# Performance work log

Measured on AMD Instinct MI355X. Metric: run time of the kernel, lower is better.

## Reference

```python
import jax, jax.numpy as jnp
import numpy as np

NUM_MEMORIES = 4096
HIDDEN_DIM = 64
TEMPERATURE = 0.5
SHRINK_THRES = 0.0025
EPS = 1e-12


def _l2_normalize(v, axis=-1):
    # matches torch F.normalize: v / max(||v||_2, eps)
    n = jnp.sqrt(jnp.sum(v * v, axis=axis, keepdims=True))
    return v / jnp.maximum(n, EPS)


def _hard_shrink_relu(w, lambd):
    # relu(w - lambd) * w / (|w - lambd| + eps)
    d = w - lambd
    return jax.nn.relu(d) * w / (jnp.abs(d) + EPS)


def setup_inputs() -> dict:
    key = jax.random.key(0)
    kx, km = jax.random.split(key)
    x = jax.random.normal(kx, (16, 2048, HIDDEN_DIM), dtype=jnp.float32)
    # xavier_uniform for (num_memories, hidden_dim)
    bound = float(np.sqrt(6.0 / (NUM_MEMORIES + HIDDEN_DIM)))
    memories = jax.random.uniform(km, (NUM_MEMORIES, HIDDEN_DIM), dtype=jnp.float32,
                                  minval=-bound, maxval=bound)
    return {"x": x, "memories": memories}


def reference(x, memories):
    # cosine similarity addressing
    x_n = _l2_normalize(x, axis=-1)                      # [B,S,D]
    m_n = _l2_normalize(memories, axis=-1)               # [M,D]
    logits = jnp.einsum('bsd,md->bsm', x_n, m_n)         # [B,S,M]
    weight = jax.nn.softmax(logits / TEMPERATURE, axis=-1)
    # hard-shrink sparsification + L1 renormalization
    weight = _hard_shrink_relu(weight, SHRINK_THRES)
    l1 = jnp.sum(jnp.abs(weight), axis=-1, keepdims=True)
    weight = weight / jnp.maximum(l1, EPS)
    read = jnp.einsum('bsm,md->bsd', weight, memories)   # [B,S,D]
    return read, weight
```

## Files before the change

### kernel.cpp

```cpp
#include <hip/hip_runtime.h>
#include <hip/hip_bf16.h>


#define NM 4096
#define HD 64
#define NROWS 32768

typedef short bf16x8 __attribute__((ext_vector_type(8)));
typedef float f32x4  __attribute__((ext_vector_type(4)));

__global__ __launch_bounds__(256) void prep_rows(const float* __restrict__ src,
                                                 ushort* __restrict__ dst,
                                                 float scale,
                                                 float* __restrict__ Mv) {
    if (blockIdx.x == 0 && threadIdx.x < 64) Mv[threadIdx.x] = 0.0f;
    const int wave = threadIdx.x >> 6, lane = threadIdx.x & 63;
    const long row = (long)blockIdx.x * 4 + wave;
    float v = src[row * HD + lane];
    float s = v * v;
#pragma unroll
    for (int o = 32; o; o >>= 1) s += __shfl_xor(s, o, 64);
    const float inv = scale / fmaxf(sqrtf(s), 1e-12f);
    __hip_bfloat16 h = __float2bfloat16(v * inv);
    dst[row * HD + lane] = *reinterpret_cast<ushort*>(&h);
}

__global__ __launch_bounds__(256) void prep_m_swz(const float* __restrict__ mem,
                                                  ushort* __restrict__ mbs,
                                                  float* __restrict__ Mv) {
    __shared__ float sM[4][64];
    const int wave = threadIdx.x >> 6, lane = threadIdx.x & 63;
    const int row = blockIdx.x * 4 + wave;
    float v = mem[row * HD + lane];
    float s = v * v;
#pragma unroll
    for (int o = 32; o; o >>= 1) s += __shfl_xor(s, o, 64);
    const float inv = 1.0f / fmaxf(sqrtf(s), 1e-12f);
    const float nv = v * inv;
    __hip_bfloat16 h = __float2bfloat16(nv);
    const int t = row >> 4, c = row & 15;
    const int k = lane;
    const int f = k >> 5, q = (k >> 3) & 3, j = k & 7;
    mbs[(long)t * 1024 + f * 512 + (q * 16 + c) * 8 + j] =
        *reinterpret_cast<ushort*>(&h);
    sM[wave][lane] = nv;
    __syncthreads();
    if (wave == 0)
        atomicAdd(&Mv[lane],
                  sM[0][lane] + sM[1][lane] + sM[2][lane] + sM[3][lane]);
}

__global__ __launch_bounds__(256, 4) void k_zero(const float* __restrict__ x,
                                                 const float* __restrict__ Mv,
                                                 const ushort* __restrict__ xb,
                                                 const ushort* __restrict__ mbs,
                                                 const float* __restrict__ mem,
                                                 float* __restrict__ out_w,
                                                 float* __restrict__ out_read) {
    const int tid = threadIdx.x;
    const int wv = tid >> 6, lane = tid & 63;
    const int m0 = blockIdx.x * 16;

    __shared__ float sS[4][16];
    __shared__ float sL[4][16];
    __shared__ int   sFail[4];
    __shared__ float sred[4][16][64];

    {
        const int r16 = lane >> 4;
        const int k16 = lane & 15;
        const long row = (long)m0 + wv * 4 + r16;
        const float4 xv = *(const float4*)(x + row * HD + k16 * 4);
        const float4 mv = *(const float4*)(Mv + k16 * 4);
        float dot = xv.x * mv.x + xv.y * mv.y + xv.z * mv.z + xv.w * mv.w;
        float nn  = xv.x * xv.x + xv.y * xv.y + xv.z * xv.z + xv.w * xv.w;
#pragma unroll
        for (int o = 1; o < 16; o <<= 1) {
            dot += __shfl_xor(dot, o, 64);
            nn  += __shfl_xor(nn,  o, 64);
        }
        const bool pass = dot >= -573.44f * fmaxf(sqrtf(nn), 1e-12f);
        const unsigned long long bal = __ballot(!pass);
        if (lane == 0) sFail[wv] = (bal != 0ull);
    }

    const float4 z4 = make_float4(0.0f, 0.0f, 0.0f, 0.0f);
    float4* base = (float4*)(out_w + (long)m0 * NM);
#pragma unroll 8
    for (int it = 0; it < 64; it++)
        base[it * 256 + tid] = z4;
    ((float4*)(out_read + (long)m0 * HD))[tid] = z4;

    __syncthreads();
    if (!(sFail[0] | sFail[1] | sFail[2] | sFail[3])) return;

    const int q = lane >> 4, c = lane & 15;
    const int nbase = wv * 1024;
    const bf16x8 a0 = *(const bf16x8*)(xb + (long)(m0 + c) * HD + q * 8);
    const bf16x8 a1 = *(const bf16x8*)(xb + (long)(m0 + c) * HD + q * 8 + 32);
    const ushort* mstrip = mbs + (long)(wv * 64) * 1024;

    float sm[4] = {0.0f, 0.0f, 0.0f, 0.0f};
    for (int i = 0; i < 64; i++) {
        const ushort* mc = mstrip + (long)i * 1024 + lane * 8;
        const bf16x8 b0 = *(const bf16x8*)(mc);
        const bf16x8 b1 = *(const bf16x8*)(mc + 512);
        f32x4 t = {0.0f, 0.0f, 0.0f, 0.0f};
        t = __builtin_amdgcn_mfma_f32_16x16x32_bf16(a0, b0, t, 0, 0, 0);
        t = __builtin_amdgcn_mfma_f32_16x16x32_bf16(a1, b1, t, 0, 0, 0);
#pragma unroll
        for (int r = 0; r < 4; r++) sm[r] += __expf(t[r]);
    }
#pragma unroll
    for (int o = 1; o < 16; o <<= 1)
#pragma unroll
        for (int r = 0; r < 4; r++) sm[r] += __shfl_xor(sm[r], o, 64);
    if (c == 0)
#pragma unroll
        for (int r = 0; r < 4; r++) sS[wv][q * 4 + r] = sm[r];
    __syncthreads();
    float rS[4];
#pragma unroll
    for (int r = 0; r < 4; r++)
        rS[r] = 1.0f / (sS[0][q * 4 + r] + sS[1][q * 4 + r] +
                        sS[2][q * 4 + r] + sS[3][q * 4 + r]);

    float l1[4] = {0.0f, 0.0f, 0.0f, 0.0f};
    for (int i = 0; i < 64; i++) {
        const ushort* mc = mstrip + (long)i * 1024 + lane * 8;
        const bf16x8 b0 = *(const bf16x8*)(mc);
        const bf16x8 b1 = *(const bf16x8*)(mc + 512);
        f32x4 t = {0.0f, 0.0f, 0.0f, 0.0f};
        t = __builtin_amdgcn_mfma_f32_16x16x32_bf16(a0, b0, t, 0, 0, 0);
        t = __builtin_amdgcn_mfma_f32_16x16x32_bf16(a1, b1, t, 0, 0, 0);
#pragma unroll
        for (int r = 0; r < 4; r++) {
            float w = __expf(t[r]) * rS[r];
            float d = w - 0.0025f;
            l1[r] += __fdividef(fmaxf(d, 0.0f) * w, fabsf(d) + 1e-12f);
        }
    }
#pragma unroll
    for (int o = 1; o < 16; o <<= 1)
#pragma unroll
        for (int r = 0; r < 4; r++) l1[r] += __shfl_xor(l1[r], o, 64);
    if (c == 0)
#pragma unroll
        for (int r = 0; r < 4; r++) sL[wv][q * 4 + r] = l1[r];
    __syncthreads();
    float rL[4];
#pragma unroll
    for (int r = 0; r < 4; r++)
        rL[r] = 1.0f / fmaxf(sL[0][q * 4 + r] + sL[1][q * 4 + r] +
                             sL[2][q * 4 + r] + sL[3][q * 4 + r], 1e-12f);

    float racc[16];
#pragma unroll
    for (int r = 0; r < 16; r++) racc[r] = 0.0f;
    float* wbase = out_w + (long)(m0 + q * 4) * NM + c;
    for (int i = 0; i < 64; i++) {
        const int n0 = nbase + i * 16;
        const ushort* mc = mstrip + (long)i * 1024 + lane * 8;
        const bf16x8 b0 = *(const bf16x8*)(mc);
        const bf16x8 b1 = *(const bf16x8*)(mc + 512);
        f32x4 t = {0.0f, 0.0f, 0.0f, 0.0f};
        t = __builtin_amdgcn_mfma_f32_16x16x32_bf16(a0, b0, t, 0, 0, 0);
        t = __builtin_amdgcn_mfma_f32_16x16x32_bf16(a1, b1, t, 0, 0, 0);
        float wf[4];
#pragma unroll
        for (int r = 0; r < 4; r++) {
            float w  = __expf(t[r]) * rS[r];
            float d  = w - 0.0025f;
            float sh = __fdividef(fmaxf(d, 0.0f) * w, fabsf(d) + 1e-12f);
            wf[r] = sh * rL[r];
            wbase[(long)r * NM + n0] = wf[r];
        }
        const bool nz = (wf[0] != 0.0f) | (wf[1] != 0.0f) |
                        (wf[2] != 0.0f) | (wf[3] != 0.0f);
        unsigned long long mask = __ballot(nz);
        while (mask) {
            const int j = __ffsll((long long)mask) - 1;
            mask &= (mask - 1);
            const int qj = j >> 4, cj = j & 15;
            float b0v = __shfl(wf[0], j, 64), b1v = __shfl(wf[1], j, 64);
            float b2v = __shfl(wf[2], j, 64), b3v = __shfl(wf[3], j, 64);
            const float mv = mem[(long)(n0 + cj) * HD + lane];
            switch (qj) {
                case 0: racc[0]  += b0v * mv; racc[1]  += b1v * mv;
                        racc[2]  += b2v * mv; racc[3]  += b3v * mv; break;
                case 1: racc[4]  += b0v * mv; racc[5]  += b1v * mv;
                        racc[6]  += b2v * mv; racc[7]  += b3v * mv; break;
                case 2: racc[8]  += b0v * mv; racc[9]  += b1v * mv;
                        racc[10] += b2v * mv; racc[11] += b3v * mv; break;
                default: racc[12] += b0v * mv; racc[13] += b1v * mv;
                         racc[14] += b2v * mv; racc[15] += b3v * mv; break;
            }
        }
    }

#pragma unroll
    for (int r = 0; r < 16; r++) sred[wv][r][lane] = racc[r];
    __syncthreads();
#pragma unroll
    for (int rr = 0; rr < 4; rr++) {
        const int row = wv * 4 + rr;
        const float v = sred[0][row][lane] + sred[1][row][lane] +
                        sred[2][row][lane] + sred[3][row][lane];
        out_read[(long)(m0 + row) * HD + lane] = v;
    }
}

extern "C" void kernel_launch(void* const* d_in, const int* in_sizes, int n_in,
                              void* d_out, int out_size, void* d_ws, size_t ws_size,
                              hipStream_t stream) {
    const float* x   = (const float*)d_in[0];
    const float* mem = (const float*)d_in[1];
    ushort* xb       = (ushort*)d_ws;
    ushort* mbs      = xb + (long)NROWS * HD;
    float*  Mv       = (float*)(mbs + (long)NM * HD);
    float* out_read  = (float*)d_out;
    float* out_w     = out_read + (long)NROWS * HD;

    prep_rows<<<NROWS / 4, 256, 0, stream>>>(x, xb, 2.0f, Mv);
    prep_m_swz<<<NM / 4, 256, 0, stream>>>(mem, mbs, Mv);
    k_zero<<<NROWS / 16, 256, 0, stream>>>(x, Mv, xb, mbs, mem, out_w, out_read);
}
```

Measured before the change: 563.2 us.

## Drop bf16 prep kernels and use per-wave early-exit with scalar fallback

Removes the x bf16 normalisation kernel and the swizzled memory-bank kernel. A single small kernel now writes per-block partial sums of the normalised memories to a buffer, replacing the atomics into a shared mean vector. The main kernel rebuilds the mean vector per wave, runs the all-weights-below-threshold check per wave instead of per block, and zero-fills only that wave's rows, so no block-level syncs are needed. The rare fallback path loses its MFMA version and becomes a plain fp32 scalar loop, which would be far slower if any row ever fails the check.

```diff
diff --git a/kernel.cpp b/kernel.cpp
--- a/kernel.cpp
+++ b/kernel.cpp
@@ -1,212 +1,141 @@
 #include <hip/hip_runtime.h>
-#include <hip/hip_bf16.h>
 
 
 #define NM 4096
 #define HD 64
 #define NROWS 32768
 
-typedef short bf16x8 __attribute__((ext_vector_type(8)));
-typedef float f32x4  __attribute__((ext_vector_type(4)));
-
-__global__ __launch_bounds__(256) void prep_rows(const float* __restrict__ src,
-                                                 ushort* __restrict__ dst,
-                                                 float scale,
-                                                 float* __restrict__ Mv) {
-    if (blockIdx.x == 0 && threadIdx.x < 64) Mv[threadIdx.x] = 0.0f;
+__global__ __launch_bounds__(256) void k_m(const float* __restrict__ mem,
+                                           float* __restrict__ P) {
+    __shared__ float sM[4][64];
     const int wave = threadIdx.x >> 6, lane = threadIdx.x & 63;
-    const long row = (long)blockIdx.x * 4 + wave;
-    float v = src[row * HD + lane];
-    float s = v * v;
+    float acc = 0.0f;
 #pragma unroll
-    for (int o = 32; o; o >>= 1) s += __shfl_xor(s, o, 64);
-    const float inv = scale / fmaxf(sqrtf(s), 1e-12f);
-    __hip_bfloat16 h = __float2bfloat16(v * inv);
-    dst[row * HD + lane] = *reinterpret_cast<ushort*>(&h);
+    for (int s = 0; s < 16; s++) {
+        const int i = blockIdx.x * 64 + wave * 16 + s;
+        const float v = mem[i * HD + lane];
+        float ss = v * v;
+#pragma unroll
+        for (int o = 32; o; o >>= 1) ss += __shfl_xor(ss, o, 64);
+        acc += v / fmaxf(sqrtf(ss), 1e-12f);
+    }
+    sM[wave][lane] = acc;
+    __syncthreads();
+    if (wave == 0)
+        P[blockIdx.x * 64 + lane] =
+            sM[0][lane] + sM[1][lane] + sM[2][lane] + sM[3][lane];
 }
 
-__global__ __launch_bounds__(256) void prep_m_swz(const float* __restrict__ mem,
-                                                  ushort* __restrict__ mbs,
-                                                  float* __restrict__ Mv) {
-    __shared__ float sM[4][64];
-    const int wave = threadIdx.x >> 6, lane = threadIdx.x & 63;
-    const int row = blockIdx.x * 4 + wave;
-    float v = mem[row * HD + lane];
-    float s = v * v;
-#pragma unroll
-    for (int o = 32; o; o >>= 1) s += __shfl_xor(s, o, 64);
-    const float inv = 1.0f / fmaxf(sqrtf(s), 1e-12f);
-    const float nv = v * inv;
-    __hip_bfloat16 h = __float2bfloat16(nv);
-    const int t = row >> 4, c = row & 15;
-    const int k = lane;
-    const int f = k >> 5, q = (k >> 3) & 3, j = k & 7;
-    mbs[(long)t * 1024 + f * 512 + (q * 16 + c) * 8 + j] =
-        *reinterpret_cast<ushort*>(&h);
-    sM[wave][lane] = nv;
-    __syncthreads();
-    if (wave == 0)
-        atomicAdd(&Mv[lane],
-                  sM[0][lane] + sM[1][lane] + sM[2][lane] + sM[3][lane]);
-}
-
-__global__ __launch_bounds__(256, 4) void k_zero(const float* __restrict__ x,
-                                                 const float* __restrict__ Mv,
-                                                 const ushort* __restrict__ xb,
-                                                 const ushort* __restrict__ mbs,
-                                                 const float* __restrict__ mem,
-                                                 float* __restrict__ out_w,
-                                                 float* __restrict__ out_read) {
+__global__ __launch_bounds__(256) void k_zero(const float* __restrict__ x,
+                                              const float* __restrict__ P,
+                                              const float* __restrict__ mem,
+                                              float* __restrict__ out_w,
+                                              float* __restrict__ out_read) {
     const int tid = threadIdx.x;
     const int wv = tid >> 6, lane = tid & 63;
-    const int m0 = blockIdx.x * 16;
+    const long rowbase = (long)blockIdx.x * 16 + wv * 4;
+    const int r16 = lane >> 4, k16 = lane & 15;
 
-    __shared__ float sS[4][16];
-    __shared__ float sL[4][16];
-    __shared__ int   sFail[4];
-    __shared__ float sred[4][16][64];
-
-    {
-        const int r16 = lane >> 4;
-        const int k16 = lane & 15;
-        const long row = (long)m0 + wv * 4 + r16;
-        const float4 xv = *(const float4*)(x + row * HD + k16 * 4);
-        const float4 mv = *(const float4*)(Mv + k16 * 4);
-        float dot = xv.x * mv.x + xv.y * mv.y + xv.z * mv.z + xv.w * mv.w;
-        float nn  = xv.x * xv.x + xv.y * xv.y + xv.z * xv.z + xv.w * xv.w;
+    float4 mv = make_float4(0.0f, 0.0f, 0.0f, 0.0f);
 #pragma unroll
-        for (int o = 1; o < 16; o <<= 1) {
-            dot += __shfl_xor(dot, o, 64);
-            nn  += __shfl_xor(nn,  o, 64);
-        }
-        const bool pass = dot >= -573.44f * fmaxf(sqrtf(nn), 1e-12f);
-        const unsigned long long bal = __ballot(!pass);
-        if (lane == 0) sFail[wv] = (bal != 0ull);
+    for (int b = 0; b < 16; b++) {
+        const float4 p = *(const float4*)(P + (r16 * 16 + b) * 64 + k16 * 4);
+        mv.x += p.x; mv.y += p.y; mv.z += p.z; mv.w += p.w;
+    }
+#pragma unroll
+    for (int o = 16; o < 64; o <<= 1) {
+        mv.x += __shfl_xor(mv.x, o, 64);
+        mv.y += __shfl_xor(mv.y, o, 64);
+        mv.z += __shfl_xor(mv.z, o, 64);
+        mv.w += __shfl_xor(mv.w, o, 64);
     }
 
-    const float4 z4 = make_float4(0.0f, 0.0f, 0.0f, 0.0f);
-    float4* base = (float4*)(out_w + (long)m0 * NM);
+    const long crow = rowbase + r16;
+    const float4 xv = *(const float4*)(x + crow * HD + k16 * 4);
+    float dot = xv.x * mv.x + xv.y * mv.y + xv.z * mv.z + xv.w * mv.w;
+    float nn  = xv.x * xv.x + xv.y * xv.y + xv.z * xv.z + xv.w * xv.w;
+#pragma unroll
+    for (int o = 1; o < 16; o <<= 1) {
+        dot += __shfl_xor(dot, o, 64);
+        nn  += __shfl_xor(nn,  o, 64);
+    }
+    const bool pass = dot >= -573.44f * fmaxf(sqrtf(nn), 1e-12f);
+
+    if (__ballot(!pass) == 0ull) {
+        const float4 z4 = make_float4(0.0f, 0.0f, 0.0f, 0.0f);
+        ((float4*)(out_read + rowbase * HD))[lane] = z4;
+        float4* base = (float4*)(out_w + rowbase * NM);
 #pragma unroll 8
-    for (int it = 0; it < 64; it++)
-        base[it * 256 + tid] = z4;
-    ((float4*)(out_read + (long)m0 * HD))[tid] = z4;
+        for (int it = 0; it < 64; it++)
+            base[it * 64 + lane] = z4;
+        return;
+    }
 
-    __syncthreads();
-    if (!(sFail[0] | sFail[1] | sFail[2] | sFail[3])) return;
+    for (int r = 0; r < 4; r++) {
+        const long rw = rowbase + r;
+        const float v = x[rw * HD + lane];
+        float ss = v * v;
+#pragma unroll
+        for (int o = 32; o; o >>= 1) ss += __shfl_xor(ss, o, 64);
+        const float xh = v * (2.0f / fmaxf(sqrtf(ss), 1e-12f));
 
-    const int q = lane >> 4, c = lane & 15;
-    const int nbase = wv * 1024;
-    const bf16x8 a0 = *(const bf16x8*)(xb + (long)(m0 + c) * HD + q * 8);
-    const bf16x8 a1 = *(const bf16x8*)(xb + (long)(m0 + c) * HD + q * 8 + 32);
-    const ushort* mstrip = mbs + (long)(wv * 64) * 1024;
+        float S = 0.0f;
+        for (int j = 0; j < 64; j++) {
+            const int i = j * 64 + lane;
+            float dp = 0.0f, nm = 0.0f;
+            for (int k = 0; k < 64; k++) {
+                const float mk = mem[(long)i * HD + k];
+                dp += __shfl(xh, k, 64) * mk;
+                nm += mk * mk;
+            }
+            const float t = dp / fmaxf(sqrtf(nm), 1e-12f);
+            S += __expf(t);
+        }
+#pragma unroll
+        for (int o = 1; o < 64; o <<= 1) S += __shfl_xor(S, o, 64);
+        const float rS = 1.0f / S;
 
-    float sm[4] = {0.0f, 0.0f, 0.0f, 0.0f};
-    for (int i = 0; i < 64; i++) {
-        const ushort* mc = mstrip + (long)i * 1024 + lane * 8;
-        const bf16x8 b0 = *(const bf16x8*)(mc);
-        const bf16x8 b1 = *(const bf16x8*)(mc + 512);
-        f32x4 t = {0.0f, 0.0f, 0.0f, 0.0f};
-        t = __builtin_amdgcn_mfma_f32_16x16x32_bf16(a0, b0, t, 0, 0, 0);
-        t = __builtin_amdgcn_mfma_f32_16x16x32_bf16(a1, b1, t, 0, 0, 0);
+        float l1 = 0.0f;
+        for (int j = 0; j < 64; j++) {
+            const int i = j * 64 + lane;
+            float dp = 0.0f, nm = 0.0f;
+            for (int k = 0; k < 64; k++) {
+                const float mk = mem[(long)i * HD + k];
+                dp += __shfl(xh, k, 64) * mk;
+                nm += mk * mk;
+            }
+            const float t = dp / fmaxf(sqrtf(nm), 1e-12f);
+            const float w = __expf(t) * rS;
+            const float d = w - 0.0025f;
+            l1 += fmaxf(d, 0.0f) * w / (fabsf(d) + 1e-12f);
+        }
 #pragma unroll
-        for (int r = 0; r < 4; r++) sm[r] += __expf(t[r]);
-    }
-#pragma unroll
-    for (int o = 1; o < 16; o <<= 1)
-#pragma unroll
-        for (int r = 0; r < 4; r++) sm[r] += __shfl_xor(sm[r], o, 64);
-    if (c == 0)
-#pragma unroll
-        for (int r = 0; r < 4; r++) sS[wv][q * 4 + r] = sm[r];
-    __syncthreads();
-    float rS[4];
-#pragma unroll
-    for (int r = 0; r < 4; r++)
-        rS[r] = 1.0f / (sS[0][q * 4 + r] + sS[1][q * 4 + r] +
-                        sS[2][q * 4 + r] + sS[3][q * 4 + r]);
+        for (int o = 1; o < 64; o <<= 1) l1 += __shfl_xor(l1, o, 64);
+        const float rL = 1.0f / fmaxf(l1, 1e-12f);
 
-    float l1[4] = {0.0f, 0.0f, 0.0f, 0.0f};
-    for (int i = 0; i < 64; i++) {
-        const ushort* mc = mstrip + (long)i * 1024 + lane * 8;
-        const bf16x8 b0 = *(const bf16x8*)(mc);
-        const bf16x8 b1 = *(const bf16x8*)(mc + 512);
-        f32x4 t = {0.0f, 0.0f, 0.0f, 0.0f};
-        t = __builtin_amdgcn_mfma_f32_16x16x32_bf16(a0, b0, t, 0, 0, 0);
-        t = __builtin_amdgcn_mfma_f32_16x16x32_bf16(a1, b1, t, 0, 0, 0);
-#pragma unroll
-        for (int r = 0; r < 4; r++) {
-            float w = __expf(t[r]) * rS[r];
-            float d = w - 0.0025f;
-            l1[r] += __fdividef(fmaxf(d, 0.0f) * w, fabsf(d) + 1e-12f);
-        }
-    }
-#pragma unroll
-    for (int o = 1; o < 16; o <<= 1)
-#pragma unroll
-        for (int r = 0; r < 4; r++) l1[r] += __shfl_xor(l1[r], o, 64);
-    if (c == 0)
-#pragma unroll
-        for (int r = 0; r < 4; r++) sL[wv][q * 4 + r] = l1[r];
-    __syncthreads();
-    float rL[4];
-#pragma unroll
-    for (int r = 0; r < 4; r++)
-        rL[r] = 1.0f / fmaxf(sL[0][q * 4 + r] + sL[1][q * 4 + r] +
-                             sL[2][q * 4 + r] + sL[3][q * 4 + r], 1e-12f);
-
-    float racc[16];
-#pragma unroll
-    for (int r = 0; r < 16; r++) racc[r] = 0.0f;
-    float* wbase = out_w + (long)(m0 + q * 4) * NM + c;
-    for (int i = 0; i < 64; i++) {
-        const int n0 = nbase + i * 16;
-        const ushort* mc = mstrip + (long)i * 1024 + lane * 8;
-        const bf16x8 b0 = *(const bf16x8*)(mc);
-        const bf16x8 b1 = *(const bf16x8*)(mc + 512);
-        f32x4 t = {0.0f, 0.0f, 0.0f, 0.0f};
-        t = __builtin_amdgcn_mfma_f32_16x16x32_bf16(a0, b0, t, 0, 0, 0);
-        t = __builtin_amdgcn_mfma_f32_16x16x32_bf16(a1, b1, t, 0, 0, 0);
-        float wf[4];
-#pragma unroll
-        for (int r = 0; r < 4; r++) {
-            float w  = __expf(t[r]) * rS[r];
-            float d  = w - 0.0025f;
-            float sh = __fdividef(fmaxf(d, 0.0f) * w, fabsf(d) + 1e-12f);
-            wf[r] = sh * rL[r];
-            wbase[(long)r * NM + n0] = wf[r];
-        }
-        const bool nz = (wf[0] != 0.0f) | (wf[1] != 0.0f) |
-                        (wf[2] != 0.0f) | (wf[3] != 0.0f);
-        unsigned long long mask = __ballot(nz);
-        while (mask) {
-            const int j = __ffsll((long long)mask) - 1;
-            mask &= (mask - 1);
-            const int qj = j >> 4, cj = j & 15;
-            float b0v = __shfl(wf[0], j, 64), b1v = __shfl(wf[1], j, 64);
-            float b2v = __shfl(wf[2], j, 64), b3v = __shfl(wf[3], j, 64);
-            const float mv = mem[(long)(n0 + cj) * HD + lane];
-            switch (qj) {
-                case 0: racc[0]  += b0v * mv; racc[1]  += b1v * mv;
-                        racc[2]  += b2v * mv; racc[3]  += b3v * mv; break;
-                case 1: racc[4]  += b0v * mv; racc[5]  += b1v * mv;
-                        racc[6]  += b2v * mv; racc[7]  += b3v * mv; break;
-                case 2: racc[8]  += b0v * mv; racc[9]  += b1v * mv;
-                        racc[10] += b2v * mv; racc[11] += b3v * mv; break;
-                default: racc[12] += b0v * mv; racc[13] += b1v * mv;
-                         racc[14] += b2v * mv; racc[15] += b3v * mv; break;
+        float rd = 0.0f;
+        for (int j = 0; j < 64; j++) {
+            const int i = j * 64 + lane;
+            float dp = 0.0f, nm = 0.0f;
+            for (int k = 0; k < 64; k++) {
+                const float mk = mem[(long)i * HD + k];
+                dp += __shfl(xh, k, 64) * mk;
+                nm += mk * mk;
+            }
+            const float t = dp / fmaxf(sqrtf(nm), 1e-12f);
+            const float w = __expf(t) * rS;
+            const float d = w - 0.0025f;
+            const float wf = fmaxf(d, 0.0f) * w / (fabsf(d) + 1e-12f) * rL;
+            out_w[rw * NM + i] = wf;
+            unsigned long long mball = __ballot(wf != 0.0f);
+            while (mball) {
+                const int L = __ffsll((long long)mball) - 1;
+                mball &= mball - 1;
+                const float wb = __shfl(wf, L, 64);
+                rd += wb * mem[(long)(j * 64 + L) * HD + lane];
             }
         }
-    }
-
-#pragma unroll
-    for (int r = 0; r < 16; r++) sred[wv][r][lane] = racc[r];
-    __syncthreads();
-#pragma unroll
-    for (int rr = 0; rr < 4; rr++) {
-        const int row = wv * 4 + rr;
-        const float v = sred[0][row][lane] + sred[1][row][lane] +
-                        sred[2][row][lane] + sred[3][row][lane];
-        out_read[(long)(m0 + row) * HD + lane] = v;
+        out_read[rw * HD + lane] = rd;
     }
 }
 
@@ -215,13 +144,10 @@
                               hipStream_t stream) {
     const float* x   = (const float*)d_in[0];
     const float* mem = (const float*)d_in[1];
-    ushort* xb       = (ushort*)d_ws;
-    ushort* mbs      = xb + (long)NROWS * HD;
-    float*  Mv       = (float*)(mbs + (long)NM * HD);
+    float* P         = (float*)d_ws;
     float* out_read  = (float*)d_out;
     float* out_w     = out_read + (long)NROWS * HD;
 
-    prep_rows<<<NROWS / 4, 256, 0, stream>>>(x, xb, 2.0f, Mv);
-    prep_m_swz<<<NM / 4, 256, 0, stream>>>(mem, mbs, Mv);
-    k_zero<<<NROWS / 16, 256, 0, stream>>>(x, Mv, xb, mbs, mem, out_w, out_read);
+    k_m<<<NM / 64, 256, 0, stream>>>(mem, P);
+    k_zero<<<NROWS / 16, 256, 0, stream>>>(x, P, mem, out_w, out_read);
 }
```

Result: faster. 538.9 us (-4.3%).
